# Optimization experiments

Measured on AMD Instinct MI355X. Metric: run time of the kernel, lower is better.

Reference implementation:

```python
import jax, jax.numpy as jnp
import numpy as np
from jax import lax

EMBED_DIM = 64
NUM_CODES = 512
NUM_HID = 128
NUM_RES_HID = 32
NUM_RES_LAYERS = 2
COMMIT_COST = 0.25
EPS = 1e-5


def conv1d(x, w, b=None, stride=1, pad=0):
    # x: [B,C,L], w: [O,I,K]
    y = lax.conv_general_dilated(x, w, (stride,), [(pad, pad)],
                                 dimension_numbers=('NCH', 'OIH', 'NCH'))
    if b is not None:
        y = y + b[None, :, None]
    return y


def conv_transpose1d(x, w, b, stride=2, pad=1):
    # torch ConvTranspose1d weight: [C_in, C_out, K]; express as fractionally-strided conv
    k = w.shape[-1]
    w2 = jnp.flip(w, axis=-1).transpose(1, 0, 2)  # [C_out, C_in, K]
    y = lax.conv_general_dilated(x, w2, (1,), [(k - 1 - pad, k - 1 - pad)],
                                 lhs_dilation=(stride,),
                                 dimension_numbers=('NCH', 'OIH', 'NCH'))
    return y + b[None, :, None]


def residual_stack(x, res_w1, res_w2):
    # res_w1: [L, R, H, 3], res_w2: [L, H, R, 1]
    for i in range(res_w1.shape[0]):
        h = conv1d(jax.nn.relu(x), res_w1[i], None, 1, 1)
        h = conv1d(jax.nn.relu(h), res_w2[i], None, 1, 0)
        x = x + h
    return jax.nn.relu(x)


def setup_inputs() -> dict:
    key = jax.random.key(0)
    ks = iter(jax.random.split(key, 32))
    B, T = 64, 8192
    H, R, D, K = NUM_HID, NUM_RES_HID, EMBED_DIM, NUM_CODES

    def w(k_, shape, fan_in):
        bound = 1.0 / np.sqrt(fan_in)
        return jax.random.uniform(k_, shape, jnp.float32, -bound, bound)

    inp = {
        'x': jax.random.normal(next(ks), (B, 1, T), jnp.float32),
        # encoder
        'enc_w1': w(next(ks), (H // 2, 1, 4), 1 * 4),
        'enc_b1': w(next(ks), (H // 2,), 1 * 4),
        'enc_w2': w(next(ks), (H, H // 2, 4), (H // 2) * 4),
        'enc_b2': w(next(ks), (H,), (H // 2) * 4),
        'enc_w3': w(next(ks), (H, H, 3), H * 3),
        'enc_b3': w(next(ks), (H,), H * 3),
        'enc_res_w1': w(next(ks), (NUM_RES_LAYERS, R, H, 3), H * 3),
        'enc_res_w2': w(next(ks), (NUM_RES_LAYERS, H, R, 1), R * 1),
        'enc_pre_w': w(next(ks), (D, H, 1), H),
        'enc_pre_b': w(next(ks), (D,), H),
        # codebook
        'codebook': jax.random.uniform(next(ks), (K, D), jnp.float32, -1.0 / K, 1.0 / K),
        # decoder
        'dec_w1': w(next(ks), (H, D, 3), D * 3),
        'dec_b1': w(next(ks), (H,), D * 3),
        'dec_res_w1': w(next(ks), (NUM_RES_LAYERS, R, H, 3), H * 3),
        'dec_res_w2': w(next(ks), (NUM_RES_LAYERS, H, R, 1), R * 1),
        'dec_t1_w': w(next(ks), (H, H // 2, 4), H * 4),   # ConvTranspose1d weight [Cin,Cout,K]
        'dec_t1_b': w(next(ks), (H // 2,), H * 4),
        'dec_t2_w': w(next(ks), (H // 2, 1, 4), (H // 2) * 4),
        'dec_t2_b': w(next(ks), (1,), (H // 2) * 4),
    }
    return inp


def vq_forward(z, codebook):
    # z: [B, D, L]
    B = z.shape[0]
    inputs = z.transpose(0, 2, 1)                       # [B, L, D]
    flat = inputs.reshape(-1, inputs.shape[-1])          # [N, D]
    # squared euclidean distances (argmin equals cdist p=2 argmin)
    d2 = (jnp.sum(flat * flat, axis=1, keepdims=True)
          - 2.0 * flat @ codebook.T
          + jnp.sum(codebook * codebook, axis=1))        # [N, K]
    idx = jnp.argmin(d2, axis=1)                         # [N]
    quant = codebook[idx].reshape(inputs.shape)          # gather == onehot @ codebook

    e_loss = jnp.mean((lax.stop_gradient(quant) - inputs) ** 2)
    q_loss = jnp.mean((quant - lax.stop_gradient(inputs)) ** 2)
    loss = q_loss + COMMIT_COST * e_loss

    quant_st = inputs + lax.stop_gradient(quant - inputs)  # straight-through

    n_tok = flat.shape[0]
    avg_probs = jnp.zeros((codebook.shape[0],), jnp.float32).at[idx].add(1.0) / n_tok
    perplexity = jnp.exp(-jnp.sum(avg_probs * jnp.log(avg_probs + 1e-10)))

    return quant_st.transpose(0, 2, 1), loss, idx.reshape(B, -1), perplexity


def reference(x, enc_w1, enc_b1, enc_w2, enc_b2, enc_w3, enc_b3,
              enc_res_w1, enc_res_w2, enc_pre_w, enc_pre_b, codebook,
              dec_w1, dec_b1, dec_res_w1, dec_res_w2,
              dec_t1_w, dec_t1_b, dec_t2_w, dec_t2_b):
    # RevIN normalize (stats detached)
    means = lax.stop_gradient(jnp.mean(x, axis=2, keepdims=True))
    stds = lax.stop_gradient(jnp.sqrt(jnp.var(x, axis=2, keepdims=True) + EPS))
    xn = (x - means) / stds

    # Encoder
    h = jax.nn.relu(conv1d(xn, enc_w1, enc_b1, 2, 1))
    h = jax.nn.relu(conv1d(h, enc_w2, enc_b2, 2, 1))
    h = conv1d(h, enc_w3, enc_b3, 1, 1)
    h = residual_stack(h, enc_res_w1, enc_res_w2)
    z = conv1d(h, enc_pre_w, enc_pre_b, 1, 0)            # [B, D, T/4]

    # VQ (eval mode: no noise, no EMA)
    quant, vq_loss, indices, perplexity = vq_forward(z, codebook)

    # Decoder
    d = conv1d(quant, dec_w1, dec_b1, 1, 1)
    d = residual_stack(d, dec_res_w1, dec_res_w2)
    d = jax.nn.relu(conv_transpose1d(d, dec_t1_w, dec_t1_b, 2, 1))
    x_recon = conv_transpose1d(d, dec_t2_w, dec_t2_b, 2, 1)

    # RevIN denormalize
    x_recon = x_recon * stds + means
    return x_recon, vq_loss, indices, perplexity
```

## Files before the change

### kernel.cpp

```cpp
#include <hip/hip_runtime.h>
#include <cmath>

#define NBATCH 64
#define TLEN   8192
#define LA     4096
#define LB     2048
#define HID    128
#define HHALF  64
#define RESCH  32
#define EMB    64
#define NCODE  512
#define NTOK   (NBATCH * LB)

#define WS_MEAN  0
#define WS_RSTD  64
#define WS_STD   128
#define WS_CNORM 192
#define WS_CNT   704
#define WS_SSE   1216
#define WS_A     4096
#define WS_B     (WS_A + 16777216)
#define WS_S     (WS_B + 16777216)


__global__ __launch_bounds__(1024) void zero_kernel(float* p, int n) {
    int i = blockIdx.x * 1024 + threadIdx.x;
    if (i < n) p[i] = 0.f;
}

__global__ __launch_bounds__(256) void cnorm_kernel(const float* __restrict__ cb,
                                                    float* __restrict__ cnorm) {
    int k = blockIdx.x * 256 + threadIdx.x;
    if (k < NCODE) {
        float p0=0,p1=0,p2=0,p3=0,p4=0,p5=0,p6=0,p7=0;
        const float* cp = cb + k * EMB;
        #pragma unroll
        for (int d = 0; d < EMB; d += 8) {
            p0 = __fadd_rn(p0, __fmul_rn(cp[d],   cp[d]));
            p1 = __fadd_rn(p1, __fmul_rn(cp[d+1], cp[d+1]));
            p2 = __fadd_rn(p2, __fmul_rn(cp[d+2], cp[d+2]));
            p3 = __fadd_rn(p3, __fmul_rn(cp[d+3], cp[d+3]));
            p4 = __fadd_rn(p4, __fmul_rn(cp[d+4], cp[d+4]));
            p5 = __fadd_rn(p5, __fmul_rn(cp[d+5], cp[d+5]));
            p6 = __fadd_rn(p6, __fmul_rn(cp[d+6], cp[d+6]));
            p7 = __fadd_rn(p7, __fmul_rn(cp[d+7], cp[d+7]));
        }
        float s01 = __fadd_rn(p0, p1), s23 = __fadd_rn(p2, p3);
        float s45 = __fadd_rn(p4, p5), s67 = __fadd_rn(p6, p7);
        cnorm[k] = __fadd_rn(__fadd_rn(s01, s23), __fadd_rn(s45, s67));
    }
}

__global__ __launch_bounds__(256) void stats_kernel(const float* __restrict__ x, float* ws) {
    __shared__ float sx[TLEN];
    __shared__ double red[256];
    const int b = blockIdx.x, t = threadIdx.x;
    const float* xb = x + (size_t)b * TLEN;
    double s = 0.0;
    for (int i = t; i < TLEN; i += 256) { float v = xb[i]; sx[i] = v; s += (double)v; }
    red[t] = s; __syncthreads();
    for (int st = 128; st > 0; st >>= 1) { if (t < st) red[t] += red[t + st]; __syncthreads(); }
    double mean = red[0] / (double)TLEN;
    __syncthreads();
    double s2 = 0.0;
    for (int i = t; i < TLEN; i += 256) { double d = (double)sx[i] - mean; s2 = fma(d, d, s2); }
    red[t] = s2; __syncthreads();
    for (int st = 128; st > 0; st >>= 1) { if (t < st) red[t] += red[t + st]; __syncthreads(); }
    if (t == 0) {
        double stdv = sqrt(red[0] / (double)TLEN + 1e-5);
        ws[WS_MEAN + b] = (float)mean;
        ws[WS_RSTD + b] = (float)(1.0 / stdv);
        ws[WS_STD + b]  = (float)stdv;
    }
}

__global__ __launch_bounds__(256) void fused12_kern(
        const float* __restrict__ x, const float* __restrict__ w1g,
        const float* __restrict__ b1g, const float* __restrict__ w2,
        const float* __restrict__ b2, const float* __restrict__ ws,
        float* __restrict__ out) {
    __shared__ float xt[262];
    __shared__ float s1e[64][65];
    __shared__ float s1o[64][65];
    __shared__ float lw1[256];
    __shared__ float lb1[64];
    const int b = blockIdx.y;
    const int l0 = blockIdx.x * 64;
    const int tid = threadIdx.x;
    const float mean = ws[WS_MEAN + b], stdv = ws[WS_STD + b];

    if (tid < 256) lw1[tid] = w1g[tid];
    if (tid < 64)  lb1[tid] = b1g[tid];
    const int x_base = 4 * l0 - 3;
    const float* xb = x + (size_t)b * TLEN;
    for (int i = tid; i < 262; i += 256) {
        int g = x_base + i;
        xt[i] = (g >= 0 && g < TLEN) ? (xb[g] - mean) / stdv : 0.f;
    }
    __syncthreads();
    for (int i = tid; i < 64 * 130; i += 256) {
        int o = i / 130, pp = i - o * 130;
        int m = 2 * l0 - 1 + pp;
        float val = 0.f;
        if (m >= 0 && m < LA) {
            float a = lb1[o];
            #pragma unroll
            for (int k = 0; k < 4; k++) a = fmaf(lw1[o * 4 + k], xt[2 * pp + k], a);
            val = fmaxf(a, 0.f);
        }
        if ((pp & 1) == 0) s1o[o][pp >> 1] = val;
        else               s1e[o][(pp - 1) >> 1] = val;
    }
    __syncthreads();
    const int lane = tid & 63;
    const int wave = tid >> 6;
    const int o0 = __builtin_amdgcn_readfirstlane(wave * 32);
    float acc[32];
    #pragma unroll
    for (int j = 0; j < 32; j++) acc[j] = b2[o0 + j];
    for (int c = 0; c < 64; c++) {
        float v0 = s1o[c][lane];
        float v1 = s1e[c][lane];
        float v2 = s1o[c][lane + 1];
        float v3 = s1e[c][lane + 1];
        #pragma unroll
        for (int j = 0; j < 32; j++) {
            const float* wp = w2 + ((size_t)(o0 + j) * 64 + c) * 4;
            float a = acc[j];
            a = fmaf(wp[0], v0, a);
            a = fmaf(wp[1], v1, a);
            a = fmaf(wp[2], v2, a);
            a = fmaf(wp[3], v3, a);
            acc[j] = a;
        }
    }
    #pragma unroll
    for (int j = 0; j < 32; j++)
        out[((size_t)b * HID + o0 + j) * LB + l0 + lane] = fmaxf(acc[j], 0.f);
}

template<int CIN, int COUT, int K, bool RELU_IN, bool RELU_OUT, bool ADD_RES, bool HAS_BIAS>
__global__ __launch_bounds__(256) void conv32_kern(
        const float* __restrict__ in, const float* __restrict__ w,
        const float* __restrict__ bias, const float* res, float* out) {
    constexpr int W = 64 + K - 1;
    __shared__ float st[CIN * W];
    const int b = blockIdx.y;
    const int l0 = blockIdx.x * 64;
    const int tid = threadIdx.x;
    const float* inb = in + (size_t)b * CIN * LB;
    for (int i = tid; i < CIN * W; i += 256) {
        int c = i / W, p = i - c * W;
        int g = l0 + p - (K / 2);
        float v = 0.f;
        if (g >= 0 && g < LB) {
            v = inb[(size_t)c * LB + g];
            if (RELU_IN) v = fmaxf(v, 0.f);
        }
        st[i] = v;
    }
    __syncthreads();
    const int lane = tid & 63;
    const int wave = tid >> 6;
    constexpr int OPW = COUT / 4;
    constexpr int NO = OPW < 16 ? OPW : 16;
    const int l = l0 + lane;
    for (int oc = 0; oc < OPW; oc += NO) {
        const int o0 = __builtin_amdgcn_readfirstlane(wave * OPW + oc);
        float acc[NO];
        #pragma unroll
        for (int j = 0; j < NO; j++) acc[j] = HAS_BIAS ? bias[o0 + j] : 0.f;
        for (int c = 0; c < CIN; c++) {
            float v[K];
            #pragma unroll
            for (int k = 0; k < K; k++) v[k] = st[c * W + lane + k];
            #pragma unroll
            for (int j = 0; j < NO; j++) {
                #pragma unroll
                for (int k = 0; k < K; k++)
                    acc[j] = fmaf(w[((o0 + j) * CIN + c) * K + k], v[k], acc[j]);
            }
        }
        #pragma unroll
        for (int j = 0; j < NO; j++) {
            float a = acc[j];
            if (ADD_RES) a += res[((size_t)b * COUT + o0 + j) * LB + l];
            if (RELU_OUT) a = fmaxf(a, 0.f);
            out[((size_t)b * COUT + o0 + j) * LB + l] = a;
        }
    }
}

__global__ __launch_bounds__(256, 2) void vq_kernel(
        const float* __restrict__ z, const float* __restrict__ cbf,
        const float* __restrict__ cnorm,
        float* __restrict__ quant, float* __restrict__ idx_out,
        float* __restrict__ cnt, float* __restrict__ sse_acc) {
    __shared__ float s_m[4][64];
    __shared__ int   s_c[4][64];
    const int tid = threadIdx.x;
    const int tl = tid & 63;
    const int q = tid >> 6;
    const int n = blockIdx.x * 64 + tl;
    const int b = n >> 11, l = n & 2047;
    const float* zp = z + (size_t)b * EMB * LB + l;
    float zv[EMB];
    #pragma unroll
    for (int d = 0; d < EMB; d++) zv[d] = zp[(size_t)d * LB];

    float p0=0,p1=0,p2=0,p3=0,p4=0,p5=0,p6=0,p7=0;
    #pragma unroll
    for (int d = 0; d < EMB; d += 8) {
        p0 = __fadd_rn(p0, __fmul_rn(zv[d],   zv[d]));
        p1 = __fadd_rn(p1, __fmul_rn(zv[d+1], zv[d+1]));
        p2 = __fadd_rn(p2, __fmul_rn(zv[d+2], zv[d+2]));
        p3 = __fadd_rn(p3, __fmul_rn(zv[d+3], zv[d+3]));
        p4 = __fadd_rn(p4, __fmul_rn(zv[d+4], zv[d+4]));
        p5 = __fadd_rn(p5, __fmul_rn(zv[d+5], zv[d+5]));
        p6 = __fadd_rn(p6, __fmul_rn(zv[d+6], zv[d+6]));
        p7 = __fadd_rn(p7, __fmul_rn(zv[d+7], zv[d+7]));
    }
    const float A = __fadd_rn(__fadd_rn(__fadd_rn(p0,p1), __fadd_rn(p2,p3)),
                              __fadd_rn(__fadd_rn(p4,p5), __fadd_rn(p6,p7)));

    const int cbase = __builtin_amdgcn_readfirstlane(q * 128);
    int coff = cbase * EMB;
    asm volatile("" : "+v"(coff));
    float m1 = 1e30f; int c1 = 0;
    for (int ci = 0; ci < 128; ci++) {
        const float* wp = cbf + coff + ci * EMB;
        float d0=0,d1=0,d2=0,d3=0,d4=0,d5=0,d6=0,d7=0;
        #pragma unroll
        for (int d = 0; d < EMB; d += 8) {
            float4 wa = *(const float4*)(wp + d);
            float4 wb = *(const float4*)(wp + d + 4);
            d0 = fmaf(wa.x, zv[d],   d0);
            d1 = fmaf(wa.y, zv[d+1], d1);
            d2 = fmaf(wa.z, zv[d+2], d2);
            d3 = fmaf(wa.w, zv[d+3], d3);
            d4 = fmaf(wb.x, zv[d+4], d4);
            d5 = fmaf(wb.y, zv[d+5], d5);
            d6 = fmaf(wb.z, zv[d+6], d6);
            d7 = fmaf(wb.w, zv[d+7], d7);
        }
        float dot = __fadd_rn(__fadd_rn(__fadd_rn(d0,d1), __fadd_rn(d2,d3)),
                              __fadd_rn(__fadd_rn(d4,d5), __fadd_rn(d6,d7)));
        float m = __fadd_rn(__fsub_rn(A, __fmul_rn(2.0f, dot)), cnorm[cbase + ci]);
        if (m < m1) { m1 = m; c1 = cbase + ci; }
    }
    s_m[q][tl] = m1; s_c[q][tl] = c1;
    __syncthreads();
    if (q == 0) {
        float bm = s_m[0][tl]; int bc = s_c[0][tl];
        #pragma unroll
        for (int qq = 1; qq < 4; qq++) {
            float mm = s_m[qq][tl];
            if (mm < bm) { bm = mm; bc = s_c[qq][tl]; }
        }
        idx_out[n] = (float)bc;
        atomicAdd(&cnt[bc], 1.0f);
        float* qp = quant + (size_t)b * EMB * LB + l;
        const float* cp = cbf + bc * EMB;
        float sse = 0.f;
        #pragma unroll
        for (int d = 0; d < EMB; d++) {
            float qv = cp[d];
            qp[(size_t)d * LB] = qv;
            float df = qv - zv[d];
            sse = fmaf(df, df, sse);
        }
        for (int off = 32; off > 0; off >>= 1) sse += __shfl_down(sse, off);
        if (tl == 0) atomicAdd(sse_acc, sse);
    }
}

__global__ __launch_bounds__(256) void convt1_kern(const float* __restrict__ in,
        const float* __restrict__ w, const float* __restrict__ bias, float* out) {
    __shared__ float s_in[HID * 66];
    const int b = blockIdx.y;
    const int t0 = blockIdx.x * 128;
    const int m0 = t0 / 2 - 1;
    const int tid = threadIdx.x;
    const float* inb = in + (size_t)b * HID * LB;
    for (int i = tid; i < HID * 66; i += 256) {
        int c = i / 66, p = i - c * 66;
        int m = m0 + p;
        s_in[i] = (m >= 0 && m < LB) ? fmaxf(inb[(size_t)c * LB + m], 0.f) : 0.f;
    }
    __syncthreads();
    const int lane = tid & 63;
    const int wave = tid >> 6;
    const int o0 = __builtin_amdgcn_readfirstlane(wave * 16);
    float accE[16], accO[16];
    #pragma unroll
    for (int j = 0; j < 16; j++) { float bv = bias[o0 + j]; accE[j] = bv; accO[j] = bv; }
    for (int c = 0; c < HID; c++) {
        float v0 = s_in[c * 66 + lane];
        float v1 = s_in[c * 66 + lane + 1];
        float v2 = s_in[c * 66 + lane + 2];
        #pragma unroll
        for (int j = 0; j < 16; j++) {
            const float* wc = w + ((size_t)c * HHALF + o0 + j) * 4;
            accE[j] = fmaf(wc[1], v1, fmaf(wc[3], v0, accE[j]));
            accO[j] = fmaf(wc[0], v2, fmaf(wc[2], v1, accO[j]));
        }
    }
    #pragma unroll
    for (int j = 0; j < 16; j++) {
        float2 pr;
        pr.x = fmaxf(accE[j], 0.f);
        pr.y = fmaxf(accO[j], 0.f);
        *(float2*)&out[((size_t)b * HHALF + o0 + j) * LA + t0 + 2 * lane] = pr;
    }
}

__global__ __launch_bounds__(256) void convt2_kern(const float* __restrict__ in,
        const float* __restrict__ w, const float* __restrict__ bias,
        const float* __restrict__ mstats, float* out) {
    __shared__ float s_in[16 * 258];
    const int b = blockIdx.y;
    const int t0 = blockIdx.x * 512;
    const int m0 = t0 / 2 - 1;
    const int tid = threadIdx.x;
    const float* inb = in + (size_t)b * HHALF * LA;
    float accE = 0.f, accO = 0.f;
    for (int cg = 0; cg < 4; cg++) {
        __syncthreads();
        for (int i = tid; i < 16 * 258; i += 256) {
            int c = i / 258, p = i - c * 258;
            int m = m0 + p;
            s_in[i] = (m >= 0 && m < LA) ? inb[(size_t)(cg * 16 + c) * LA + m] : 0.f;
        }
        __syncthreads();
        for (int c = 0; c < 16; c++) {
            float v0 = s_in[c * 258 + tid];
            float v1 = s_in[c * 258 + tid + 1];
            float v2 = s_in[c * 258 + tid + 2];
            const float* wc = w + (size_t)(cg * 16 + c) * 4;
            accE = fmaf(wc[1], v1, fmaf(wc[3], v0, accE));
            accO = fmaf(wc[0], v2, fmaf(wc[2], v1, accO));
        }
    }
    const float mean = mstats[WS_MEAN + b], stdv = mstats[WS_STD + b];
    const float b0 = bias[0];
    float2 pr;
    pr.x = (accE + b0) * stdv + mean;
    pr.y = (accO + b0) * stdv + mean;
    *(float2*)&out[(size_t)b * TLEN + t0 + 2 * tid] = pr;
}

__global__ __launch_bounds__(512) void finalize_kernel(const float* cnt, const float* sse,
                                                       float* d_out) {
    __shared__ float red[512];
    const int t = threadIdx.x;
    float n = cnt[t];
    float p = n / (float)NTOK;
    red[t] = -p * logf(p + 1e-10f);
    __syncthreads();
    for (int s = 256; s > 0; s >>= 1) { if (t < s) red[t] += red[t + s]; __syncthreads(); }
    if (t == 0) {
        d_out[(size_t)NBATCH * TLEN] = sse[0] * 1.25f / (float)((size_t)NTOK * EMB);
        d_out[(size_t)NBATCH * TLEN + 1 + NTOK] = expf(red[0]);
    }
}

extern "C" void kernel_launch(void* const* d_in, const int* in_sizes, int n_in,
                              void* d_out, int out_size, void* d_ws, size_t ws_size,
                              hipStream_t stream) {
    (void)in_sizes; (void)n_in; (void)out_size; (void)ws_size;

    const float* x         = (const float*)d_in[0];
    const float* enc_w1    = (const float*)d_in[1];
    const float* enc_b1    = (const float*)d_in[2];
    const float* enc_w2    = (const float*)d_in[3];
    const float* enc_b2    = (const float*)d_in[4];
    const float* enc_w3    = (const float*)d_in[5];
    const float* enc_b3    = (const float*)d_in[6];
    const float* enc_rw1   = (const float*)d_in[7];
    const float* enc_rw2   = (const float*)d_in[8];
    const float* enc_pre_w = (const float*)d_in[9];
    const float* enc_pre_b = (const float*)d_in[10];
    const float* codebook  = (const float*)d_in[11];
    const float* dec_w1    = (const float*)d_in[12];
    const float* dec_b1    = (const float*)d_in[13];
    const float* dec_rw1   = (const float*)d_in[14];
    const float* dec_rw2   = (const float*)d_in[15];
    const float* dec_t1_w  = (const float*)d_in[16];
    const float* dec_t1_b  = (const float*)d_in[17];
    const float* dec_t2_w  = (const float*)d_in[18];
    const float* dec_t2_b  = (const float*)d_in[19];

    float* ws  = (float*)d_ws;
    float* out = (float*)d_out;
    float* A   = ws + WS_A;
    float* Bb  = ws + WS_B;
    float* S   = ws + WS_S;
    float* z     = Bb;
    float* quant = Bb + (size_t)NBATCH * EMB * LB;
    float* idx_out = out + (size_t)NBATCH * TLEN + 1;

    zero_kernel<<<1, 1024, 0, stream>>>(ws + WS_CNT, 513);
    cnorm_kernel<<<2, 256, 0, stream>>>(codebook, ws + WS_CNORM);
    stats_kernel<<<NBATCH, 256, 0, stream>>>(x, ws);

    fused12_kern<<<dim3(LB / 64, NBATCH), 256, 0, stream>>>(x, enc_w1, enc_b1,
                                                            enc_w2, enc_b2, ws, Bb);
    conv32_kern<128, 128, 3, false, false, false, true>
        <<<dim3(LB / 64, NBATCH), 256, 0, stream>>>(Bb, enc_w3, enc_b3, nullptr, A);
    for (int i = 0; i < 2; i++) {
        conv32_kern<128, 32, 3, true, false, false, false>
            <<<dim3(LB / 64, NBATCH), 256, 0, stream>>>(A, enc_rw1 + (size_t)i * RESCH * HID * 3,
                                                        nullptr, nullptr, S);
        conv32_kern<32, 128, 1, true, false, true, false>
            <<<dim3(LB / 64, NBATCH), 256, 0, stream>>>(S, enc_rw2 + (size_t)i * HID * RESCH,
                                                        nullptr, A, A);
    }
    conv32_kern<128, 64, 1, true, false, false, true>
        <<<dim3(LB / 64, NBATCH), 256, 0, stream>>>(A, enc_pre_w, enc_pre_b, nullptr, z);

    vq_kernel<<<NTOK / 64, 256, 0, stream>>>(z, codebook, ws + WS_CNORM,
                                             quant, idx_out, ws + WS_CNT, ws + WS_SSE);

    conv32_kern<64, 128, 3, false, false, false, true>
        <<<dim3(LB / 64, NBATCH), 256, 0, stream>>>(quant, dec_w1, dec_b1, nullptr, A);
    for (int i = 0; i < 2; i++) {
        conv32_kern<128, 32, 3, true, false, false, false>
            <<<dim3(LB / 64, NBATCH), 256, 0, stream>>>(A, dec_rw1 + (size_t)i * RESCH * HID * 3,
                                                        nullptr, nullptr, S);
        conv32_kern<32, 128, 1, true, false, true, false>
            <<<dim3(LB / 64, NBATCH), 256, 0, stream>>>(S, dec_rw2 + (size_t)i * HID * RESCH,
                                                        nullptr, A, A);
    }
    convt1_kern<<<dim3(LA / 128, NBATCH), 256, 0, stream>>>(A, dec_t1_w, dec_t1_b, Bb);
    convt2_kern<<<dim3(TLEN / 512, NBATCH), 256, 0, stream>>>(Bb, dec_t2_w, dec_t2_b, ws, out);

    finalize_kernel<<<1, 512, 0, stream>>>(ws + WS_CNT, ws + WS_SSE, out);
}
```

Baseline: 3.599 ms.

## Stage codebook chunks in LDS and assign one token per thread in VQ

Replaces the per-wave codebook split with a per-thread full scan over all codes, loading the codebook into shared memory in 64-code chunks with block-wide syncs. This removes the cross-wave argmin merge and lets all 256 threads do the quantize/SSE epilogue. The occupancy hint rises to 4 blocks per CU. The trade-offs are per-thread work growing fourfold, extra barriers, and possible register pressure or spills given the 64-float register array.

```diff
diff --git a/kernel.cpp b/kernel.cpp
--- a/kernel.cpp
+++ b/kernel.cpp
@@ -191,17 +191,17 @@
     }
 }
 
-__global__ __launch_bounds__(256, 2) void vq_kernel(
+#define VQ_CHUNK 64
+__global__ __launch_bounds__(256, 4) void vq_kernel(
         const float* __restrict__ z, const float* __restrict__ cbf,
         const float* __restrict__ cnorm,
         float* __restrict__ quant, float* __restrict__ idx_out,
         float* __restrict__ cnt, float* __restrict__ sse_acc) {
-    __shared__ float s_m[4][64];
-    __shared__ int   s_c[4][64];
+    __shared__ float s_cb[VQ_CHUNK * EMB];
+    __shared__ float s_cn[VQ_CHUNK];
     const int tid = threadIdx.x;
-    const int tl = tid & 63;
-    const int q = tid >> 6;
-    const int n = blockIdx.x * 64 + tl;
+    const int lane = tid & 63;
+    const int n = blockIdx.x * 256 + tid;
     const int b = n >> 11, l = n & 2047;
     const float* zp = z + (size_t)b * EMB * LB + l;
     float zv[EMB];
@@ -223,55 +223,54 @@
     const float A = __fadd_rn(__fadd_rn(__fadd_rn(p0,p1), __fadd_rn(p2,p3)),
                               __fadd_rn(__fadd_rn(p4,p5), __fadd_rn(p6,p7)));
 
-    const int cbase = __builtin_amdgcn_readfirstlane(q * 128);
-    int coff = cbase * EMB;
-    asm volatile("" : "+v"(coff));
     float m1 = 1e30f; int c1 = 0;
-    for (int ci = 0; ci < 128; ci++) {
-        const float* wp = cbf + coff + ci * EMB;
-        float d0=0,d1=0,d2=0,d3=0,d4=0,d5=0,d6=0,d7=0;
-        #pragma unroll
-        for (int d = 0; d < EMB; d += 8) {
-            float4 wa = *(const float4*)(wp + d);
-            float4 wb = *(const float4*)(wp + d + 4);
-            d0 = fmaf(wa.x, zv[d],   d0);
-            d1 = fmaf(wa.y, zv[d+1], d1);
-            d2 = fmaf(wa.z, zv[d+2], d2);
-            d3 = fmaf(wa.w, zv[d+3], d3);
-            d4 = fmaf(wb.x, zv[d+4], d4);
-            d5 = fmaf(wb.y, zv[d+5], d5);
-            d6 = fmaf(wb.z, zv[d+6], d6);
-            d7 = fmaf(wb.w, zv[d+7], d7);
-        }
-        float dot = __fadd_rn(__fadd_rn(__fadd_rn(d0,d1), __fadd_rn(d2,d3)),
-                              __fadd_rn(__fadd_rn(d4,d5), __fadd_rn(d6,d7)));
-        float m = __fadd_rn(__fsub_rn(A, __fmul_rn(2.0f, dot)), cnorm[cbase + ci]);
-        if (m < m1) { m1 = m; c1 = cbase + ci; }
-    }
-    s_m[q][tl] = m1; s_c[q][tl] = c1;
-    __syncthreads();
-    if (q == 0) {
-        float bm = s_m[0][tl]; int bc = s_c[0][tl];
-        #pragma unroll
-        for (int qq = 1; qq < 4; qq++) {
-            float mm = s_m[qq][tl];
-            if (mm < bm) { bm = mm; bc = s_c[qq][tl]; }
-        }
-        idx_out[n] = (float)bc;
-        atomicAdd(&cnt[bc], 1.0f);
-        float* qp = quant + (size_t)b * EMB * LB + l;
-        const float* cp = cbf + bc * EMB;
-        float sse = 0.f;
-        #pragma unroll
-        for (int d = 0; d < EMB; d++) {
-            float qv = cp[d];
-            qp[(size_t)d * LB] = qv;
-            float df = qv - zv[d];
-            sse = fmaf(df, df, sse);
-        }
-        for (int off = 32; off > 0; off >>= 1) sse += __shfl_down(sse, off);
-        if (tl == 0) atomicAdd(sse_acc, sse);
-    }
+    for (int ch = 0; ch < NCODE / VQ_CHUNK; ch++) {
+        __syncthreads();
+        {
+            const float4* src = (const float4*)(cbf + (size_t)ch * VQ_CHUNK * EMB);
+            float4* dst = (float4*)s_cb;
+            #pragma unroll
+            for (int i = 0; i < (VQ_CHUNK * EMB / 4) / 256; i++)
+                dst[tid + i * 256] = src[tid + i * 256];
+            if (tid < VQ_CHUNK) s_cn[tid] = cnorm[ch * VQ_CHUNK + tid];
+        }
+        __syncthreads();
+        for (int cc = 0; cc < VQ_CHUNK; cc++) {
+            const float* wp = s_cb + cc * EMB;
+            float d0=0,d1=0,d2=0,d3=0,d4=0,d5=0,d6=0,d7=0;
+            #pragma unroll
+            for (int d = 0; d < EMB; d += 8) {
+                float4 wa = *(const float4*)(wp + d);
+                float4 wb = *(const float4*)(wp + d + 4);
+                d0 = fmaf(wa.x, zv[d],   d0);
+                d1 = fmaf(wa.y, zv[d+1], d1);
+                d2 = fmaf(wa.z, zv[d+2], d2);
+                d3 = fmaf(wa.w, zv[d+3], d3);
+                d4 = fmaf(wb.x, zv[d+4], d4);
+                d5 = fmaf(wb.y, zv[d+5], d5);
+                d6 = fmaf(wb.z, zv[d+6], d6);
+                d7 = fmaf(wb.w, zv[d+7], d7);
+            }
+            float dot = __fadd_rn(__fadd_rn(__fadd_rn(d0,d1), __fadd_rn(d2,d3)),
+                                  __fadd_rn(__fadd_rn(d4,d5), __fadd_rn(d6,d7)));
+            float m = __fadd_rn(__fsub_rn(A, __fmul_rn(2.0f, dot)), s_cn[cc]);
+            if (m < m1) { m1 = m; c1 = ch * VQ_CHUNK + cc; }
+        }
+    }
+    idx_out[n] = (float)c1;
+    atomicAdd(&cnt[c1], 1.0f);
+    float* qp = quant + (size_t)b * EMB * LB + l;
+    const float* cp = cbf + (size_t)c1 * EMB;
+    float sse = 0.f;
+    #pragma unroll
+    for (int d = 0; d < EMB; d++) {
+        float qv = cp[d];
+        qp[(size_t)d * LB] = qv;
+        float df = qv - zv[d];
+        sse = fmaf(df, df, sse);
+    }
+    for (int off = 32; off > 0; off >>= 1) sse += __shfl_down(sse, off);
+    if (lane == 0) atomicAdd(sse_acc, sse);
 }
 
 __global__ __launch_bounds__(256) void convt1_kern(const float* __restrict__ in,
@@ -418,8 +417,8 @@
     conv32_kern<128, 64, 1, true, false, false, true>
         <<<dim3(LB / 64, NBATCH), 256, 0, stream>>>(A, enc_pre_w, enc_pre_b, nullptr, z);
 
-    vq_kernel<<<NTOK / 64, 256, 0, stream>>>(z, codebook, ws + WS_CNORM,
-                                             quant, idx_out, ws + WS_CNT, ws + WS_SSE);
+    vq_kernel<<<NTOK / 256, 256, 0, stream>>>(z, codebook, ws + WS_CNORM,
+                                              quant, idx_out, ws + WS_CNT, ws + WS_SSE);
 
     conv32_kern<64, 128, 3, false, false, false, true>
         <<<dim3(LB / 64, NBATCH), 256, 0, stream>>>(quant, dec_w1, dec_b1, nullptr, A);
```

Result: no change. 3.582 ms (-0.5%).
